# Performance work log

Hardware: AMD Instinct MI355X
Metric: run time of the kernel (lower is better)

## Reference

```python
import jax, jax.numpy as jnp
import numpy as np

NUM_HEAD = 16
DIM_HEAD = 64
SCALE = DIM_HEAD ** -0.5


def setup_inputs() -> dict:
    key = jax.random.key(0)
    k1, k2, k3 = jax.random.split(key, 3)
    B, N, D = 4, 2048, 1024
    x = jax.random.normal(k1, (B, N, D), dtype=jnp.float32)
    w_qkv = jax.random.normal(k2, (D, 3 * NUM_HEAD * DIM_HEAD), dtype=jnp.float32) * (D ** -0.5)
    w_out = jax.random.normal(k3, (NUM_HEAD * DIM_HEAD, D), dtype=jnp.float32) * ((NUM_HEAD * DIM_HEAD) ** -0.5)
    return {"x": x, "w_qkv": w_qkv, "w_out": w_out}


def reference(x, w_qkv, w_out):
    B, N, D = x.shape
    qkv = x @ w_qkv  # [B, N, 3*H*Dh]
    q, k, v = jnp.split(qkv, 3, axis=-1)
    def heads(t):
        return t.reshape(B, N, NUM_HEAD, DIM_HEAD).transpose(0, 2, 1, 3)  # b h n d
    q, k, v = heads(q), heads(k), heads(v)
    scores = jnp.einsum('bhnd,bhmd->bhnm', q, k) * SCALE
    attn = jax.nn.softmax(scores, axis=-1)
    out = jnp.einsum('bhnm,bhmd->bhnd', attn, v)
    out = out.transpose(0, 2, 1, 3).reshape(B, N, NUM_HEAD * DIM_HEAD)
    return out @ w_out
```

## Files before the change

### kernel.cpp

```cpp
#include <hip/hip_runtime.h>
#include <hip/hip_bf16.h>
#include <stdint.h>


typedef __attribute__((ext_vector_type(8))) __bf16 bf16x8;
typedef __attribute__((ext_vector_type(4))) __bf16 bf16x4;
typedef __attribute__((ext_vector_type(4))) float f32x4;
typedef __attribute__((ext_vector_type(16))) float f32x16;
typedef __attribute__((ext_vector_type(4))) unsigned int u32x4;

#define EXPC 0.18033688011112042f
#define THRR 64.0f

static __device__ __forceinline__ void gload_lds16(const void* g, void* s) {
  __builtin_amdgcn_global_load_lds(
      (__attribute__((address_space(1))) unsigned int*)g,
      (__attribute__((address_space(3))) unsigned int*)s, 16, 0, 0);
}

static __device__ __forceinline__ unsigned pk2(float lo, float hi) {
  unsigned short a = __builtin_bit_cast(unsigned short, (__bf16)lo);
  unsigned short b = __builtin_bit_cast(unsigned short, (__bf16)hi);
  return (unsigned)a | ((unsigned)b << 16);
}

__global__ void k_cvt(const float* __restrict__ src, __bf16* __restrict__ dst, int n4) {
  int i = blockIdx.x * blockDim.x + threadIdx.x;
  if (i >= n4) return;
  float4 v = reinterpret_cast<const float4*>(src)[i];
  bf16x4 o = { (__bf16)v.x, (__bf16)v.y, (__bf16)v.z, (__bf16)v.w };
  *reinterpret_cast<bf16x4*>(dst + (size_t)i * 4) = o;
}

__global__ void k_tcvt(const float* __restrict__ src, __bf16* __restrict__ dst, int W, int Hs) {
  __shared__ float tile[32][33];
  int tx = threadIdx.x, ty = threadIdx.y;
  int x = blockIdx.x * 32 + tx;
  int y0 = blockIdx.y * 32;
  for (int j = ty; j < 32; j += 8) tile[j][tx] = src[(size_t)(y0 + j) * W + x];
  __syncthreads();
  int xo = y0 + tx;
  int yo = blockIdx.x * 32;
  for (int j = ty; j < 32; j += 8) dst[(size_t)(yo + j) * Hs + xo] = (__bf16)tile[tx][j];
}

static __device__ __forceinline__ void gemm_core(
    const __bf16* __restrict__ A, const __bf16* __restrict__ BT, int K,
    int m0, int n0, f32x4 acc[4][4], __bf16* As, __bf16* Bs) {
  const int tid = threadIdx.x;
  const int lane = tid & 63, w = tid >> 6;
  const int fr = lane & 15, fq = lane >> 4;
  const int srow = lane >> 2, scol = (lane & 3) * 8;
  const int wr = (w >> 1) * 64, wc = (w & 1) * 64;
#pragma unroll
  for (int mi = 0; mi < 4; ++mi)
#pragma unroll
    for (int nj = 0; nj < 4; ++nj) acc[mi][nj] = (f32x4){0.f, 0.f, 0.f, 0.f};

  for (int ko = 0; ko < K; ko += 32) {
#pragma unroll
    for (int i = 0; i < 2; ++i) {
      int rb = w * 32 + i * 16;
      gload_lds16(A + (size_t)(m0 + rb + srow) * K + ko + scol, As + rb * 32);
      gload_lds16(BT + (size_t)(n0 + rb + srow) * K + ko + scol, Bs + rb * 32);
    }
    __syncthreads();
    bf16x8 af[4], bfv[4];
#pragma unroll
    for (int mi = 0; mi < 4; ++mi)
      af[mi] = *(const bf16x8*)(As + (wr + mi * 16 + fr) * 32 + fq * 8);
#pragma unroll
    for (int nj = 0; nj < 4; ++nj)
      bfv[nj] = *(const bf16x8*)(Bs + (wc + nj * 16 + fr) * 32 + fq * 8);
#pragma unroll
    for (int mi = 0; mi < 4; ++mi)
#pragma unroll
      for (int nj = 0; nj < 4; ++nj)
        acc[mi][nj] = __builtin_amdgcn_mfma_f32_16x16x32_bf16(af[mi], bfv[nj], acc[mi][nj], 0, 0, 0);
    __syncthreads();
  }
}

__global__ __launch_bounds__(256) void k_gemm_qkv(
    const __bf16* __restrict__ A, const __bf16* __restrict__ BT,
    __bf16* __restrict__ qb, __bf16* __restrict__ kb, __bf16* __restrict__ vb) {
  __shared__ __align__(16) __bf16 As[128 * 32];
  __shared__ __align__(16) __bf16 Bs[128 * 32];
  f32x4 acc[4][4];
  int m0 = blockIdx.x * 128, n0 = blockIdx.y * 128;
  gemm_core(A, BT, 1024, m0, n0, acc, As, Bs);
  const int lane = threadIdx.x & 63, w = threadIdx.x >> 6;
  const int fr = lane & 15, fq = lane >> 4;
  const int wr = (w >> 1) * 64, wc = (w & 1) * 64;
  const int which = n0 >> 10;
#pragma unroll
  for (int mi = 0; mi < 4; ++mi) {
#pragma unroll
    for (int nj = 0; nj < 4; ++nj) {
      int row = m0 + wr + mi * 16 + fq * 4;
      int col = n0 + wc + nj * 16 + fr;
      int rem = col & 1023, h = rem >> 6, d = rem & 63;
      int bb = row >> 11, n = row & 2047;
      int bh = bb * 16 + h;
      if (which == 2) {
        bf16x4 pk = { (__bf16)acc[mi][nj][0], (__bf16)acc[mi][nj][1],
                      (__bf16)acc[mi][nj][2], (__bf16)acc[mi][nj][3] };
        *reinterpret_cast<bf16x4*>(vb + ((size_t)bh * 64 + d) * 2048 + n) = pk;
      } else {
        __bf16* dst = (which == 0) ? qb : kb;
#pragma unroll
        for (int j = 0; j < 4; ++j)
          dst[((size_t)bh * 2048 + (n + j)) * 64 + d] = (__bf16)acc[mi][nj][j];
      }
    }
  }
}

__global__ __launch_bounds__(256) void k_gemm_out(
    const __bf16* __restrict__ A, const __bf16* __restrict__ BT, float* __restrict__ C) {
  __shared__ __align__(16) __bf16 As[128 * 32];
  __shared__ __align__(16) __bf16 Bs[128 * 32];
  f32x4 acc[4][4];
  int m0 = blockIdx.x * 128, n0 = blockIdx.y * 128;
  gemm_core(A, BT, 1024, m0, n0, acc, As, Bs);
  const int lane = threadIdx.x & 63, w = threadIdx.x >> 6;
  const int fr = lane & 15, fq = lane >> 4;
  const int wr = (w >> 1) * 64, wc = (w & 1) * 64;
#pragma unroll
  for (int mi = 0; mi < 4; ++mi)
#pragma unroll
    for (int nj = 0; nj < 4; ++nj)
#pragma unroll
      for (int j = 0; j < 4; ++j)
        C[(size_t)(m0 + wr + mi * 16 + fq * 4 + j) * 1024 + n0 + wc + nj * 16 + fr] =
            acc[mi][nj][j];
}

__global__ __launch_bounds__(512, 1) void k_attn(
    const __bf16* __restrict__ qb, const __bf16* __restrict__ kb,
    const __bf16* __restrict__ vb, __bf16* __restrict__ ao) {
  __shared__ __align__(16) __bf16 Ks[2][64 * 64];
  __shared__ __align__(16) __bf16 Vs[2][64 * 64];
  const int tid = threadIdx.x, lane = tid & 63, w = tid >> 6;
  const int r31 = lane & 31, hi = lane >> 5;
  const int lsw = (lane & 7) ^ ((lane >> 3) & 3);
  const int bh = blockIdx.x & 63, qblk = blockIdx.x >> 6;
  const __bf16* kbase = kb + (size_t)bh * 2048 * 64;
  const __bf16* vbase = vb + (size_t)bh * 64 * 2048;

  const int srow = tid >> 3;
  const int ssc = (tid & 7) ^ (srow & 7) ^ ((srow >> 3) & 3);
  const int wid = tid >> 6;

  const int nbase = qblk * 256 + w * 32;
  const __bf16* qptr = qb + ((size_t)bh * 2048 + nbase + r31) * 64;
  bf16x8 qf[4];
#pragma unroll
  for (int dd = 0; dd < 4; ++dd)
    qf[dd] = *(const bf16x8*)(qptr + dd * 16 + hi * 8);

  f32x16 o0, o1;
#pragma unroll
  for (int r = 0; r < 16; ++r) { o0[r] = 0.f; o1[r] = 0.f; }
  float m = -1e30f, lsum = 0.f;

  auto stage = [&](int buf, int j0) {
    gload_lds16(kbase + (size_t)(j0 + srow) * 64 + ssc * 8, &Ks[buf][wid * 512]);
    gload_lds16(vbase + (size_t)srow * 2048 + j0 + ssc * 8, &Vs[buf][wid * 512]);
  };

  stage(0, 0);
  __syncthreads();

  for (int kt = 0; kt < 32; ++kt) {
    const int cur = kt & 1;
    if (kt < 31) stage(cur ^ 1, (kt + 1) * 64);

    f32x16 sa0, sa1;
#pragma unroll
    for (int r = 0; r < 16; ++r) { sa0[r] = 0.f; sa1[r] = 0.f; }
    __builtin_amdgcn_s_setprio(1);
#pragma unroll
    for (int dd = 0; dd < 4; ++dd) {
      bf16x8 k0 = *(const bf16x8*)(&Ks[cur][r31 * 64 + (((dd * 2 + hi) ^ lsw) << 3)]);
      bf16x8 k1 = *(const bf16x8*)(&Ks[cur][(32 + r31) * 64 + (((dd * 2 + hi) ^ lsw) << 3)]);
      sa0 = __builtin_amdgcn_mfma_f32_32x32x16_bf16(k0, qf[dd], sa0, 0, 0, 0);
      sa1 = __builtin_amdgcn_mfma_f32_32x32x16_bf16(k1, qf[dd], sa1, 0, 0, 0);
    }
    __builtin_amdgcn_s_setprio(0);

    float pmax = sa0[0];
#pragma unroll
    for (int r = 1; r < 16; ++r) pmax = fmaxf(pmax, sa0[r]);
#pragma unroll
    for (int r = 0; r < 16; ++r) pmax = fmaxf(pmax, sa1[r]);
    pmax = fmaxf(pmax, __shfl_xor(pmax, 32, 64));

    if (!__all(pmax - m <= THRR)) {
      float mn = fmaxf(m, pmax);
      float corr = __builtin_amdgcn_exp2f((m - mn) * EXPC);
      m = mn;
      lsum *= corr;
#pragma unroll
      for (int r = 0; r < 16; ++r) {
        int qrow = (r & 3) + 8 * (r >> 2) + 4 * hi;
        float cr = __shfl(corr, qrow, 64);
        o0[r] *= cr; o1[r] *= cr;
      }
    }

    const float mc = m * EXPC;
    float p[2][16];
    float rs = 0.f;
#pragma unroll
    for (int r = 0; r < 16; ++r) {
      p[0][r] = __builtin_amdgcn_exp2f(fmaf(sa0[r], EXPC, -mc));
      p[1][r] = __builtin_amdgcn_exp2f(fmaf(sa1[r], EXPC, -mc));
      rs += p[0][r] + p[1][r];
    }
    lsum += rs;

    unsigned f[4][4];
#pragma unroll
    for (int kb2 = 0; kb2 < 2; ++kb2) {
#pragma unroll
      for (int ks = 0; ks < 2; ++ks) {
        unsigned a0 = pk2(p[kb2][ks * 8 + 0], p[kb2][ks * 8 + 1]);
        unsigned a1 = pk2(p[kb2][ks * 8 + 2], p[kb2][ks * 8 + 3]);
        unsigned b0 = pk2(p[kb2][ks * 8 + 4], p[kb2][ks * 8 + 5]);
        unsigned b1 = pk2(p[kb2][ks * 8 + 6], p[kb2][ks * 8 + 7]);
        asm("v_permlane32_swap_b32 %0, %1" : "+v"(a0), "+v"(b0));
        asm("v_permlane32_swap_b32 %0, %1" : "+v"(a1), "+v"(b1));
        f[kb2 * 2 + ks][0] = a0; f[kb2 * 2 + ks][1] = a1;
        f[kb2 * 2 + ks][2] = b0; f[kb2 * 2 + ks][3] = b1;
      }
    }

    __builtin_amdgcn_s_setprio(1);
#pragma unroll
    for (int kk = 0; kk < 4; ++kk) {
      u32x4 fw = {f[kk][0], f[kk][1], f[kk][2], f[kk][3]};
      bf16x8 pa = __builtin_bit_cast(bf16x8, fw);
      bf16x8 v0 = *(const bf16x8*)(&Vs[cur][r31 * 64 + (((kk * 2 + hi) ^ lsw) << 3)]);
      bf16x8 v1 = *(const bf16x8*)(&Vs[cur][(32 + r31) * 64 + (((kk * 2 + hi) ^ lsw) << 3)]);
      o0 = __builtin_amdgcn_mfma_f32_32x32x16_bf16(pa, v0, o0, 0, 0, 0);
      o1 = __builtin_amdgcn_mfma_f32_32x32x16_bf16(pa, v1, o1, 0, 0, 0);
    }
    __builtin_amdgcn_s_setprio(0);

    __syncthreads();
  }

  lsum += __shfl_xor(lsum, 32, 64);
  float inv = 1.0f / lsum;
  const int b = bh >> 4, h = bh & 15;
  __bf16* abase = ao + ((size_t)b * 2048 + nbase) * 1024 + h * 64 + r31;
#pragma unroll
  for (int r = 0; r < 16; ++r) {
    int qrow = (r & 3) + 8 * (r >> 2) + 4 * hi;
    float ir = __shfl(inv, qrow, 64);
    abase[(size_t)qrow * 1024] = (__bf16)(o0[r] * ir);
    abase[(size_t)qrow * 1024 + 32] = (__bf16)(o1[r] * ir);
  }
}

extern "C" void kernel_launch(void* const* d_in, const int* in_sizes, int n_in,
                              void* d_out, int out_size, void* d_ws, size_t ws_size,
                              hipStream_t stream) {
  (void)in_sizes; (void)n_in; (void)out_size; (void)ws_size;
  const float* x = (const float*)d_in[0];
  const float* w_qkv = (const float*)d_in[1];
  const float* w_out = (const float*)d_in[2];
  float* out = (float*)d_out;

  char* p = (char*)d_ws;
  __bf16* xb    = (__bf16*)p; p += (size_t)8192 * 1024 * 2;
  __bf16* wqkvT = (__bf16*)p; p += (size_t)3072 * 1024 * 2;
  __bf16* woutT = (__bf16*)p; p += (size_t)1024 * 1024 * 2;
  __bf16* qb    = (__bf16*)p; p += (size_t)64 * 2048 * 64 * 2;
  __bf16* kb    = (__bf16*)p; p += (size_t)64 * 2048 * 64 * 2;
  __bf16* vb    = (__bf16*)p; p += (size_t)64 * 64 * 2048 * 2;
  __bf16* ao    = (__bf16*)p; p += (size_t)8192 * 1024 * 2;

  k_cvt<<<8192, 256, 0, stream>>>(x, xb, 2097152);
  k_tcvt<<<dim3(96, 32), dim3(32, 8), 0, stream>>>(w_qkv, wqkvT, 3072, 1024);
  k_tcvt<<<dim3(32, 32), dim3(32, 8), 0, stream>>>(w_out, woutT, 1024, 1024);
  k_gemm_qkv<<<dim3(64, 24), 256, 0, stream>>>(xb, wqkvT, qb, kb, vb);
  k_attn<<<dim3(512), dim3(512), 0, stream>>>(qb, kb, vb, ao);
  k_gemm_out<<<dim3(64, 8), 256, 0, stream>>>(ao, woutT, out);
}
```

Before: 222.0 us.

## Split attention blocks to 256 threads and tree-reduce row max and sum

The attention kernel now launches 1024 blocks of 256 threads (4 waves, 128 query rows) with launch bounds allowing 2 blocks per CU, instead of 512 blocks of 512 threads. K/V staging is reorganized so each thread issues two LDS-direct loads per tile to cover the 64-row tile with fewer threads. The per-tile row max and row sum are computed with pairwise tree reductions instead of serial chains, which shortens dependency chains. The intent is better CU load balance and occupancy, at the cost of each K/V tile being loaded by twice as many blocks.

Result: faster. 217.0 us (-2.3%).

```diff
diff --git a/kernel.cpp b/kernel.cpp
--- a/kernel.cpp
+++ b/kernel.cpp
@@ -136,23 +136,19 @@
             acc[mi][nj][j];
 }
 
-__global__ __launch_bounds__(512, 1) void k_attn(
+__global__ __launch_bounds__(256, 2) void k_attn(
     const __bf16* __restrict__ qb, const __bf16* __restrict__ kb,
     const __bf16* __restrict__ vb, __bf16* __restrict__ ao) {
   __shared__ __align__(16) __bf16 Ks[2][64 * 64];
   __shared__ __align__(16) __bf16 Vs[2][64 * 64];
-  const int tid = threadIdx.x, lane = tid & 63, w = tid >> 6;
+  const int tid = threadIdx.x, lane = tid & 63, wid = tid >> 6;
   const int r31 = lane & 31, hi = lane >> 5;
   const int lsw = (lane & 7) ^ ((lane >> 3) & 3);
   const int bh = blockIdx.x & 63, qblk = blockIdx.x >> 6;
   const __bf16* kbase = kb + (size_t)bh * 2048 * 64;
   const __bf16* vbase = vb + (size_t)bh * 64 * 2048;
 
-  const int srow = tid >> 3;
-  const int ssc = (tid & 7) ^ (srow & 7) ^ ((srow >> 3) & 3);
-  const int wid = tid >> 6;
-
-  const int nbase = qblk * 256 + w * 32;
+  const int nbase = qblk * 128 + wid * 32;
   const __bf16* qptr = qb + ((size_t)bh * 2048 + nbase + r31) * 64;
   bf16x8 qf[4];
 #pragma unroll
@@ -165,8 +161,14 @@
   float m = -1e30f, lsum = 0.f;
 
   auto stage = [&](int buf, int j0) {
-    gload_lds16(kbase + (size_t)(j0 + srow) * 64 + ssc * 8, &Ks[buf][wid * 512]);
-    gload_lds16(vbase + (size_t)srow * 2048 + j0 + ssc * 8, &Vs[buf][wid * 512]);
+#pragma unroll
+    for (int p2 = 0; p2 < 2; ++p2) {
+      int row = p2 * 32 + (tid >> 3);
+      int sc = (tid & 7) ^ (row & 7) ^ ((row >> 3) & 3);
+      int dst = p2 * 2048 + wid * 512;
+      gload_lds16(kbase + (size_t)(j0 + row) * 64 + sc * 8, &Ks[buf][dst]);
+      gload_lds16(vbase + (size_t)row * 2048 + j0 + sc * 8, &Vs[buf][dst]);
+    }
   };
 
   stage(0, 0);
@@ -189,12 +191,15 @@
     }
     __builtin_amdgcn_s_setprio(0);
 
-    float pmax = sa0[0];
-#pragma unroll
-    for (int r = 1; r < 16; ++r) pmax = fmaxf(pmax, sa0[r]);
-#pragma unroll
-    for (int r = 0; r < 16; ++r) pmax = fmaxf(pmax, sa1[r]);
-    pmax = fmaxf(pmax, __shfl_xor(pmax, 32, 64));
+    float mx[8];
+#pragma unroll
+    for (int r = 0; r < 8; ++r)
+      mx[r] = fmaxf(fmaxf(sa0[2 * r], sa0[2 * r + 1]), fmaxf(sa1[2 * r], sa1[2 * r + 1]));
+#pragma unroll
+    for (int s = 4; s > 0; s >>= 1)
+#pragma unroll
+      for (int r = 0; r < s; ++r) mx[r] = fmaxf(mx[r], mx[r + s]);
+    float pmax = fmaxf(mx[0], __shfl_xor(mx[0], 32, 64));
 
     if (!__all(pmax - m <= THRR)) {
       float mn = fmaxf(m, pmax);
@@ -211,14 +216,20 @@
 
     const float mc = m * EXPC;
     float p[2][16];
-    float rs = 0.f;
 #pragma unroll
     for (int r = 0; r < 16; ++r) {
       p[0][r] = __builtin_amdgcn_exp2f(fmaf(sa0[r], EXPC, -mc));
       p[1][r] = __builtin_amdgcn_exp2f(fmaf(sa1[r], EXPC, -mc));
-      rs += p[0][r] + p[1][r];
-    }
-    lsum += rs;
+    }
+    float ss[8];
+#pragma unroll
+    for (int r = 0; r < 8; ++r)
+      ss[r] = (p[0][2 * r] + p[0][2 * r + 1]) + (p[1][2 * r] + p[1][2 * r + 1]);
+#pragma unroll
+    for (int s = 4; s > 0; s >>= 1)
+#pragma unroll
+      for (int r = 0; r < s; ++r) ss[r] += ss[r + s];
+    lsum += ss[0];
 
     unsigned f[4][4];
 #pragma unroll
@@ -286,6 +297,6 @@
   k_tcvt<<<dim3(96, 32), dim3(32, 8), 0, stream>>>(w_qkv, wqkvT, 3072, 1024);
   k_tcvt<<<dim3(32, 32), dim3(32, 8), 0, stream>>>(w_out, woutT, 1024, 1024);
   k_gemm_qkv<<<dim3(64, 24), 256, 0, stream>>>(xb, wqkvT, qb, kb, vb);
-  k_attn<<<dim3(512), dim3(512), 0, stream>>>(qb, kb, vb, ao);
+  k_attn<<<dim3(1024), dim3(256), 0, stream>>>(qb, kb, vb, ao);
   k_gemm_out<<<dim3(64, 8), 256, 0, stream>>>(ao, woutT, out);
 }
```
